# Kernel optimization log

Measured on AMD Instinct MI355X. Metric: run time of the kernel, lower is better.

The kernel has to match this reference:

```python
import jax, jax.numpy as jnp
import numpy as np

B, TD, SD, H = 512, 2048, 768, 128


def setup_inputs() -> dict:
    key = jax.random.key(0)
    ks = jax.random.split(key, 12)
    s = lambda k, shape, fan_in: jax.random.normal(k, shape, jnp.float32) * (1.0 / np.sqrt(fan_in))
    return {
        "teacher_features": jax.random.normal(ks[0], (B, TD), jnp.float32),
        "student_features": jax.random.normal(ks[1], (B, SD), jnp.float32),
        # Linear weights stored [in, out] (transposed vs torch) so y = x @ W + b
        "Wt": s(ks[2], (TD, H), TD), "bt": jnp.zeros((H,), jnp.float32),
        "Ws": s(ks[3], (SD, H), SD), "bs": jnp.zeros((H,), jnp.float32),
        "W1": s(ks[4], (2 * H, H), 2 * H), "b1": jnp.zeros((H,), jnp.float32),
        "W2": s(ks[5], (H, 1), H), "b2": jnp.zeros((1,), jnp.float32),
    }


def reference(teacher_features, student_features, Wt, bt, Ws, bs, W1, b1, W2, b2):
    def compute_relations(f):
        b, h = f.shape
        # pairwise concat [f_i, f_j] -> [B, B, 2H]
        pair = jnp.concatenate(
            [jnp.broadcast_to(f[:, None, :], (b, b, h)),
             jnp.broadcast_to(f[None, :, :], (b, b, h))], axis=-1)
        hdn = jax.nn.relu(jnp.einsum('ijk,kh->ijh', pair, W1) + b1)
        rel = jax.nn.sigmoid(jnp.einsum('ijh,ho->ijo', hdn, W2) + b2)[..., 0]
        # diagonal stays zero (i != j in the original loop)
        return rel * (1.0 - jnp.eye(b, dtype=rel.dtype))

    tp = teacher_features @ Wt + bt  # [B, H]
    sp = student_features @ Ws + bs  # [B, H]
    t_rel = compute_relations(tp)
    s_rel = compute_relations(sp)
    return jnp.mean((s_rel - t_rel) ** 2)
```

## Files before the change

### kernel.cpp

```cpp
#include <hip/hip_runtime.h>

#define HDIM 128
#define BDIM 512

typedef __attribute__((ext_vector_type(8))) __bf16 bf16x8;
typedef __attribute__((ext_vector_type(4))) float  f32x4;

__global__ __launch_bounds__(256) void proj_mfma(
    const float* __restrict__ Ft, const float* __restrict__ Fs,
    const float* __restrict__ Wt, const float* __restrict__ Ws,
    __bf16* __restrict__ Pbt, __bf16* __restrict__ Pbs)
{
    const int tid = threadIdx.x;
    const int wv = tid >> 6, l = tid & 63;
    const int t = blockIdx.x;
    const int net = t >> 8;
    const int mtile = (t >> 3) & 31, ntile = t & 7;

    const float* F; const float* W; __bf16* P; int K;
    if (net == 0) { F = Ft; W = Wt; P = Pbt; K = 2048; }
    else          { F = Fs; W = Ws; P = Pbs; K = 768;  }

    const int m0 = mtile * 16, n0 = ntile * 16;
    const int Ks = K >> 2;
    const int q = l >> 4, ln = l & 15;
    const int arow = m0 + ln;
    const int bn = n0 + ln;

    f32x4 acc = {0.f, 0.f, 0.f, 0.f};
    for (int k0 = wv * Ks; k0 < (wv + 1) * Ks; k0 += 32) {
        const int ka = k0 + q * 8;
        const float4 fa0 = *(const float4*)&F[(size_t)arow * K + ka];
        const float4 fa1 = *(const float4*)&F[(size_t)arow * K + ka + 4];
        bf16x8 a, b;
        a[0] = (__bf16)fa0.x; a[1] = (__bf16)fa0.y; a[2] = (__bf16)fa0.z; a[3] = (__bf16)fa0.w;
        a[4] = (__bf16)fa1.x; a[5] = (__bf16)fa1.y; a[6] = (__bf16)fa1.z; a[7] = (__bf16)fa1.w;
        #pragma unroll
        for (int j = 0; j < 8; ++j)
            b[j] = (__bf16)W[(size_t)(ka + j) * HDIM + bn];
        acc = __builtin_amdgcn_mfma_f32_16x16x32_bf16(a, b, acc, 0, 0, 0);
    }

    __shared__ float lds[4 * 256];
    #pragma unroll
    for (int r = 0; r < 4; ++r) lds[wv * 256 + r * 64 + l] = acc[r];
    __syncthreads();

    {
        const float s = lds[tid] + lds[256 + tid] + lds[512 + tid] + lds[768 + tid];
        const int r = tid >> 6, l2 = tid & 63;
        const int row = m0 + ((l2 >> 4) << 2) + r;
        const int col = n0 + (l2 & 15);
        P[(size_t)row * HDIM + col] = (__bf16)s;
    }
}

__global__ __launch_bounds__(64) void uv_mfma(
    const __bf16* __restrict__ Pbt, const __bf16* __restrict__ Pbs,
    const float* __restrict__ bt, const float* __restrict__ bs,
    const float* __restrict__ W1, const float* __restrict__ b1,
    float* __restrict__ Ut, float* __restrict__ Vt,
    float* __restrict__ Us, float* __restrict__ Vs,
    float* __restrict__ out)
{
    const int t = blockIdx.x;
    const int net = t >> 9, uvh = (t >> 8) & 1;
    const int mtile = (t >> 3) & 31, ntile = t & 7;
    const int l = threadIdx.x;

    if (t == 0 && l == 0) out[0] = 0.f;

    const __bf16* P   = net ? Pbs : Pbt;
    const float* bias = net ? bs : bt;
    float* O = net ? (uvh ? Vs : Us) : (uvh ? Vt : Ut);
    const float* W1o = W1 + (size_t)uvh * HDIM * HDIM;

    const int m0 = mtile * 16, n0 = ntile * 16;
    const int q = l >> 4, ln = l & 15;
    const int arow = m0 + ln, bn = n0 + ln;

    f32x4 acc = {0.f, 0.f, 0.f, 0.f};
    float cpart = 0.f;
    #pragma unroll
    for (int k0 = 0; k0 < HDIM; k0 += 32) {
        const int ka = k0 + q * 8;
        bf16x8 a = *(const bf16x8*)&P[(size_t)arow * HDIM + ka];
        bf16x8 b;
        #pragma unroll
        for (int j = 0; j < 8; ++j) {
            const float w = W1o[(size_t)(ka + j) * HDIM + bn];
            b[j] = (__bf16)w;
            cpart = fmaf(bias[ka + j], w, cpart);
        }
        acc = __builtin_amdgcn_mfma_f32_16x16x32_bf16(a, b, acc, 0, 0, 0);
    }
    cpart += __shfl_xor(cpart, 16, 64);
    cpart += __shfl_xor(cpart, 32, 64);
    const float cfull = cpart + (uvh == 0 ? b1[bn] : 0.f);

    #pragma unroll
    for (int r = 0; r < 4; ++r) {
        const int row = m0 + q * 4 + r;
        O[(size_t)row * HDIM + bn] = acc[r] + cfull;
    }
}

__global__ __launch_bounds__(256) void pair_kernel(
    const float* __restrict__ Ut, const float* __restrict__ Vt,
    const float* __restrict__ Us, const float* __restrict__ Vs,
    const float* __restrict__ W2, const float* __restrict__ b2,
    float* __restrict__ out)
{
    __shared__ alignas(16) float4 tUt[32 * 17];
    __shared__ alignas(16) float4 tVt[32 * 17];
    __shared__ alignas(16) float4 tUs[32 * 17];
    __shared__ alignas(16) float4 tVs[32 * 17];
    __shared__ alignas(16) float4 w2s[32];
    __shared__ float red[256];

    const int tx = threadIdx.x, ty = threadIdx.y;
    const int tid = ty * 16 + tx;
    const int i0 = blockIdx.y * 32, j0 = blockIdx.x * 32;

    const float4* Ut4 = (const float4*)Ut;
    const float4* Vt4 = (const float4*)Vt;
    const float4* Us4 = (const float4*)Us;
    const float4* Vs4 = (const float4*)Vs;

    if (tid < 32) w2s[tid] = ((const float4*)W2)[tid];

    float aT[2][2] = {{0.f, 0.f}, {0.f, 0.f}};
    float aS[2][2] = {{0.f, 0.f}, {0.f, 0.f}};

    for (int half = 0; half < 2; ++half) {
        const int c0 = half * 16;
        __syncthreads();
        #pragma unroll
        for (int it = 0; it < 2; ++it) {
            int fi = tid + 256 * it;
            int r = fi >> 4, c = fi & 15;
            tUt[r * 17 + c] = Ut4[(size_t)(i0 + r) * 32 + c0 + c];
            tVt[r * 17 + c] = Vt4[(size_t)(j0 + r) * 32 + c0 + c];
            tUs[r * 17 + c] = Us4[(size_t)(i0 + r) * 32 + c0 + c];
            tVs[r * 17 + c] = Vs4[(size_t)(j0 + r) * 32 + c0 + c];
        }
        __syncthreads();

        #pragma unroll 4
        for (int h4 = 0; h4 < 16; ++h4) {
            float4 w = w2s[c0 + h4];
            float4 u[2], v[2], p[2], q[2];
            u[0] = tUt[ty * 17 + h4];        u[1] = tUt[(ty + 16) * 17 + h4];
            v[0] = tVt[tx * 17 + h4];        v[1] = tVt[(tx + 16) * 17 + h4];
            p[0] = tUs[ty * 17 + h4];        p[1] = tUs[(ty + 16) * 17 + h4];
            q[0] = tVs[tx * 17 + h4];        q[1] = tVs[(tx + 16) * 17 + h4];
            #pragma unroll
            for (int a = 0; a < 2; ++a)
                #pragma unroll
                for (int b = 0; b < 2; ++b) {
                    aT[a][b] = fmaf(fmaxf(u[a].x + v[b].x, 0.f), w.x,
                               fmaf(fmaxf(u[a].y + v[b].y, 0.f), w.y,
                               fmaf(fmaxf(u[a].z + v[b].z, 0.f), w.z,
                               fmaf(fmaxf(u[a].w + v[b].w, 0.f), w.w, aT[a][b]))));
                    aS[a][b] = fmaf(fmaxf(p[a].x + q[b].x, 0.f), w.x,
                               fmaf(fmaxf(p[a].y + q[b].y, 0.f), w.y,
                               fmaf(fmaxf(p[a].z + q[b].z, 0.f), w.z,
                               fmaf(fmaxf(p[a].w + q[b].w, 0.f), w.w, aS[a][b]))));
                }
        }
    }

    const float b2v = b2[0];
    float local = 0.f;
    #pragma unroll
    for (int a = 0; a < 2; ++a)
        #pragma unroll
        for (int b = 0; b < 2; ++b) {
            int i = i0 + ty + 16 * a;
            int j = j0 + tx + 16 * b;
            if (i != j) {
                float tr = 1.f / (1.f + __expf(-(aT[a][b] + b2v)));
                float sr = 1.f / (1.f + __expf(-(aS[a][b] + b2v)));
                float d = sr - tr;
                local = fmaf(d, d, local);
            }
        }

    red[tid] = local;
    __syncthreads();
    #pragma unroll
    for (int s = 128; s > 0; s >>= 1) {
        if (tid < s) red[tid] += red[tid + s];
        __syncthreads();
    }
    if (tid == 0)
        atomicAdd(out, red[0] * (1.0f / ((float)BDIM * (float)BDIM)));
}

extern "C" void kernel_launch(void* const* d_in, const int* in_sizes, int n_in,
                              void* d_out, int out_size, void* d_ws, size_t ws_size,
                              hipStream_t stream) {
    const float* teacher = (const float*)d_in[0];
    const float* student = (const float*)d_in[1];
    const float* Wt = (const float*)d_in[2];
    const float* bt = (const float*)d_in[3];
    const float* Ws = (const float*)d_in[4];
    const float* bs = (const float*)d_in[5];
    const float* W1 = (const float*)d_in[6];
    const float* b1 = (const float*)d_in[7];
    const float* W2 = (const float*)d_in[8];
    const float* b2 = (const float*)d_in[9];
    float* out = (float*)d_out;

    const size_t M = (size_t)BDIM * HDIM;
    __bf16* Pbt = (__bf16*)d_ws;
    __bf16* Pbs = Pbt + M;
    float* Ut = (float*)(Pbs + M);
    float* Vt = Ut + M;
    float* Us = Vt + M;
    float* Vs = Us + M;

    proj_mfma<<<512, 256, 0, stream>>>(teacher, student, Wt, Ws, Pbt, Pbs);

    uv_mfma<<<1024, 64, 0, stream>>>(Pbt, Pbs, bt, bs, W1, b1,
                                     Ut, Vt, Us, Vs, out);

    pair_kernel<<<dim3(16, 16), dim3(16, 16), 0, stream>>>(
        Ut, Vt, Us, Vs, W2, b2, out);
}
```

Measured before the change: 100.6 us.

## Template projection K for full unroll, remap block order, double pair-kernel threads

```diff
diff --git a/kernel.cpp b/kernel.cpp
--- a/kernel.cpp
+++ b/kernel.cpp
@@ -6,40 +6,52 @@
 typedef __attribute__((ext_vector_type(8))) __bf16 bf16x8;
 typedef __attribute__((ext_vector_type(4))) float  f32x4;
 
-__global__ __launch_bounds__(256) void proj_mfma(
-    const float* __restrict__ Ft, const float* __restrict__ Fs,
-    const float* __restrict__ Wt, const float* __restrict__ Ws,
-    __bf16* __restrict__ Pbt, __bf16* __restrict__ Pbs)
-{
-    const int tid = threadIdx.x;
-    const int wv = tid >> 6, l = tid & 63;
-    const int t = blockIdx.x;
-    const int net = t >> 8;
-    const int mtile = (t >> 3) & 31, ntile = t & 7;
-
-    const float* F; const float* W; __bf16* P; int K;
-    if (net == 0) { F = Ft; W = Wt; P = Pbt; K = 2048; }
-    else          { F = Fs; W = Ws; P = Pbs; K = 768;  }
-
-    const int m0 = mtile * 16, n0 = ntile * 16;
-    const int Ks = K >> 2;
+template<int K>
+__device__ __forceinline__ f32x4 proj_acc(const float* __restrict__ F,
+                                          const float* __restrict__ W,
+                                          int m0, int n0, int wv, int l)
+{
+    constexpr int Ks = K >> 2;
     const int q = l >> 4, ln = l & 15;
-    const int arow = m0 + ln;
-    const int bn = n0 + ln;
-
+    const float* Fp = &F[(size_t)(m0 + ln) * K + wv * Ks + q * 8];
+    const float* Wp = &W[(size_t)(wv * Ks + q * 8) * HDIM + n0 + ln];
     f32x4 acc = {0.f, 0.f, 0.f, 0.f};
-    for (int k0 = wv * Ks; k0 < (wv + 1) * Ks; k0 += 32) {
-        const int ka = k0 + q * 8;
-        const float4 fa0 = *(const float4*)&F[(size_t)arow * K + ka];
-        const float4 fa1 = *(const float4*)&F[(size_t)arow * K + ka + 4];
+    #pragma unroll
+    for (int k0 = 0; k0 < Ks; k0 += 32) {
+        const float4 fa0 = *(const float4*)(Fp + k0);
+        const float4 fa1 = *(const float4*)(Fp + k0 + 4);
         bf16x8 a, b;
         a[0] = (__bf16)fa0.x; a[1] = (__bf16)fa0.y; a[2] = (__bf16)fa0.z; a[3] = (__bf16)fa0.w;
         a[4] = (__bf16)fa1.x; a[5] = (__bf16)fa1.y; a[6] = (__bf16)fa1.z; a[7] = (__bf16)fa1.w;
         #pragma unroll
         for (int j = 0; j < 8; ++j)
-            b[j] = (__bf16)W[(size_t)(ka + j) * HDIM + bn];
+            b[j] = (__bf16)Wp[(size_t)(k0 + j) * HDIM];
         acc = __builtin_amdgcn_mfma_f32_16x16x32_bf16(a, b, acc, 0, 0, 0);
     }
+    return acc;
+}
+
+__global__ __launch_bounds__(256) void proj_mfma(
+    const float* __restrict__ Ft, const float* __restrict__ Fs,
+    const float* __restrict__ Wt, const float* __restrict__ Ws,
+    __bf16* __restrict__ Pbt, __bf16* __restrict__ Pbs)
+{
+    const int tid = threadIdx.x;
+    const int wv = tid >> 6, l = tid & 63;
+
+    const int bid = blockIdx.x;
+    const int c  = bid & 7;
+    const int tt = bid >> 3;
+    const int ntile = tt & 7;
+    const int g  = ((tt >> 3) << 3) + c;
+    const int net = g >> 5, mtile = g & 31;
+
+    const int m0 = mtile * 16, n0 = ntile * 16;
+
+    f32x4 acc;
+    __bf16* P;
+    if (net == 0) { acc = proj_acc<2048>(Ft, Wt, m0, n0, wv, l); P = Pbt; }
+    else          { acc = proj_acc<768 >(Fs, Ws, m0, n0, wv, l); P = Pbs; }
 
     __shared__ float lds[4 * 256];
     #pragma unroll
@@ -105,7 +117,7 @@
     }
 }
 
-__global__ __launch_bounds__(256) void pair_kernel(
+__global__ __launch_bounds__(512) void pair_kernel(
     const float* __restrict__ Ut, const float* __restrict__ Vt,
     const float* __restrict__ Us, const float* __restrict__ Vs,
     const float* __restrict__ W2, const float* __restrict__ b2,
@@ -116,7 +128,7 @@
     __shared__ alignas(16) float4 tUs[32 * 17];
     __shared__ alignas(16) float4 tVs[32 * 17];
     __shared__ alignas(16) float4 w2s[32];
-    __shared__ float red[256];
+    __shared__ float red[512];
 
     const int tx = threadIdx.x, ty = threadIdx.y;
     const int tid = ty * 16 + tx;
@@ -129,67 +141,68 @@
 
     if (tid < 32) w2s[tid] = ((const float4*)W2)[tid];
 
-    float aT[2][2] = {{0.f, 0.f}, {0.f, 0.f}};
-    float aS[2][2] = {{0.f, 0.f}, {0.f, 0.f}};
+    float aT[2] = {0.f, 0.f};
+    float aS[2] = {0.f, 0.f};
 
     for (int half = 0; half < 2; ++half) {
         const int c0 = half * 16;
         __syncthreads();
-        #pragma unroll
-        for (int it = 0; it < 2; ++it) {
-            int fi = tid + 256 * it;
-            int r = fi >> 4, c = fi & 15;
-            tUt[r * 17 + c] = Ut4[(size_t)(i0 + r) * 32 + c0 + c];
-            tVt[r * 17 + c] = Vt4[(size_t)(j0 + r) * 32 + c0 + c];
-            tUs[r * 17 + c] = Us4[(size_t)(i0 + r) * 32 + c0 + c];
-            tVs[r * 17 + c] = Vs4[(size_t)(j0 + r) * 32 + c0 + c];
+        {
+            const int r = tid >> 4, cc = tid & 15;
+            tUt[r * 17 + cc] = Ut4[(size_t)(i0 + r) * 32 + c0 + cc];
+            tVt[r * 17 + cc] = Vt4[(size_t)(j0 + r) * 32 + c0 + cc];
+            tUs[r * 17 + cc] = Us4[(size_t)(i0 + r) * 32 + c0 + cc];
+            tVs[r * 17 + cc] = Vs4[(size_t)(j0 + r) * 32 + c0 + cc];
         }
         __syncthreads();
 
         #pragma unroll 4
         for (int h4 = 0; h4 < 16; ++h4) {
-            float4 w = w2s[c0 + h4];
-            float4 u[2], v[2], p[2], q[2];
-            u[0] = tUt[ty * 17 + h4];        u[1] = tUt[(ty + 16) * 17 + h4];
-            v[0] = tVt[tx * 17 + h4];        v[1] = tVt[(tx + 16) * 17 + h4];
-            p[0] = tUs[ty * 17 + h4];        p[1] = tUs[(ty + 16) * 17 + h4];
-            q[0] = tVs[tx * 17 + h4];        q[1] = tVs[(tx + 16) * 17 + h4];
-            #pragma unroll
-            for (int a = 0; a < 2; ++a)
-                #pragma unroll
-                for (int b = 0; b < 2; ++b) {
-                    aT[a][b] = fmaf(fmaxf(u[a].x + v[b].x, 0.f), w.x,
-                               fmaf(fmaxf(u[a].y + v[b].y, 0.f), w.y,
-                               fmaf(fmaxf(u[a].z + v[b].z, 0.f), w.z,
-                               fmaf(fmaxf(u[a].w + v[b].w, 0.f), w.w, aT[a][b]))));
-                    aS[a][b] = fmaf(fmaxf(p[a].x + q[b].x, 0.f), w.x,
-                               fmaf(fmaxf(p[a].y + q[b].y, 0.f), w.y,
-                               fmaf(fmaxf(p[a].z + q[b].z, 0.f), w.z,
-                               fmaf(fmaxf(p[a].w + q[b].w, 0.f), w.w, aS[a][b]))));
-                }
+            float4 w  = w2s[c0 + h4];
+            float4 u  = tUt[ty * 17 + h4];
+            float4 p  = tUs[ty * 17 + h4];
+            float4 v0 = tVt[tx * 17 + h4];
+            float4 v1 = tVt[(tx + 16) * 17 + h4];
+            float4 q0 = tVs[tx * 17 + h4];
+            float4 q1 = tVs[(tx + 16) * 17 + h4];
+
+            aT[0] = fmaf(fmaxf(u.x + v0.x, 0.f), w.x,
+                    fmaf(fmaxf(u.y + v0.y, 0.f), w.y,
+                    fmaf(fmaxf(u.z + v0.z, 0.f), w.z,
+                    fmaf(fmaxf(u.w + v0.w, 0.f), w.w, aT[0]))));
+            aT[1] = fmaf(fmaxf(u.x + v1.x, 0.f), w.x,
+                    fmaf(fmaxf(u.y + v1.y, 0.f), w.y,
+                    fmaf(fmaxf(u.z + v1.z, 0.f), w.z,
+                    fmaf(fmaxf(u.w + v1.w, 0.f), w.w, aT[1]))));
+            aS[0] = fmaf(fmaxf(p.x + q0.x, 0.f), w.x,
+                    fmaf(fmaxf(p.y + q0.y, 0.f), w.y,
+                    fmaf(fmaxf(p.z + q0.z, 0.f), w.z,
+                    fmaf(fmaxf(p.w + q0.w, 0.f), w.w, aS[0]))));
+            aS[1] = fmaf(fmaxf(p.x + q1.x, 0.f), w.x,
+                    fmaf(fmaxf(p.y + q1.y, 0.f), w.y,
+                    fmaf(fmaxf(p.z + q1.z, 0.f), w.z,
+                    fmaf(fmaxf(p.w + q1.w, 0.f), w.w, aS[1]))));
         }
     }
 
     const float b2v = b2[0];
     float local = 0.f;
     #pragma unroll
-    for (int a = 0; a < 2; ++a)
-        #pragma unroll
-        for (int b = 0; b < 2; ++b) {
-            int i = i0 + ty + 16 * a;
-            int j = j0 + tx + 16 * b;
-            if (i != j) {
-                float tr = 1.f / (1.f + __expf(-(aT[a][b] + b2v)));
-                float sr = 1.f / (1.f + __expf(-(aS[a][b] + b2v)));
-                float d = sr - tr;
-                local = fmaf(d, d, local);
-            }
-        }
+    for (int b = 0; b < 2; ++b) {
+        const int i = i0 + ty;
+        const int j = j0 + tx + 16 * b;
+        if (i != j) {
+            float tr = 1.f / (1.f + __expf(-(aT[b] + b2v)));
+            float sr = 1.f / (1.f + __expf(-(aS[b] + b2v)));
+            float d = sr - tr;
+            local = fmaf(d, d, local);
+        }
+    }
 
     red[tid] = local;
     __syncthreads();
     #pragma unroll
-    for (int s = 128; s > 0; s >>= 1) {
+    for (int s = 256; s > 0; s >>= 1) {
         if (tid < s) red[tid] += red[tid + s];
         __syncthreads();
     }
@@ -225,6 +238,6 @@
     uv_mfma<<<1024, 64, 0, stream>>>(Pbt, Pbs, bt, bs, W1, b1,
                                      Ut, Vt, Us, Vs, out);
 
-    pair_kernel<<<dim3(16, 16), dim3(16, 16), 0, stream>>>(
+    pair_kernel<<<dim3(16, 16), dim3(16, 32), 0, stream>>>(
         Ut, Vt, Us, Vs, W2, b2, out);
 }
```

New measurement: 97.11 us. 3.5% less time.
